# Kernel tuning notes

Measured on AMD Instinct MI355X. Metric: run time of the kernel, lower is better.

Reference implementation:

```python
import jax, jax.numpy as jnp
import numpy as np

B, S, D, H = 2, 2048, 1024, 16
DK = D // H


def setup_inputs() -> dict:
    key = jax.random.key(0)
    ks = jax.random.split(key, 12)
    scale = 0.02
    inp = {
        "query": jax.random.normal(ks[0], (B, S, D), jnp.float32),
        "key_": jax.random.normal(ks[1], (B, S, D), jnp.float32),
        "value": jax.random.normal(ks[2], (B, S, D), jnp.float32),
        # causal mask; masked_fill where mask == 0
        "mask": jnp.tril(jnp.ones((S, S), jnp.int32))[None, None, :, :],
        # torch Linear weights are [out, in]; y = x @ W.T + b
        "Wq": jax.random.normal(ks[3], (D, D), jnp.float32) * scale,
        "bq": jax.random.normal(ks[4], (D,), jnp.float32) * scale,
        "Wk": jax.random.normal(ks[5], (D, D), jnp.float32) * scale,
        "bk": jax.random.normal(ks[6], (D,), jnp.float32) * scale,
        "Wv": jax.random.normal(ks[7], (D, D), jnp.float32) * scale,
        "bv": jax.random.normal(ks[8], (D,), jnp.float32) * scale,
        "Wo": jax.random.normal(ks[9], (D, D), jnp.float32) * scale,
        "bo": jax.random.normal(ks[10], (D,), jnp.float32) * scale,
    }
    return inp


def reference(query, key_, value, mask, Wq, bq, Wk, bk, Wv, bv, Wo, bo):
    # projections (torch Linear: x @ W.T + b)
    Q = query @ Wq.T + bq
    K = key_ @ Wk.T + bk
    V = value @ Wv.T + bv
    # [B, S, D] -> [B, H, S, DK]
    Q = Q.reshape(B, S, H, DK).transpose(0, 2, 1, 3)
    K = K.reshape(B, S, H, DK).transpose(0, 2, 1, 3)
    V = V.reshape(B, S, H, DK).transpose(0, 2, 1, 3)
    scores = jnp.einsum("bhqd,bhkd->bhqk", Q, K) / jnp.sqrt(jnp.float32(DK))
    scores = jnp.where(mask == 0, jnp.float32(-1e9), scores)
    attn = jax.nn.softmax(scores, axis=-1)
    # dropout is identity in eval mode
    context = jnp.einsum("bhqk,bhkd->bhqd", attn, V)
    context = context.transpose(0, 2, 1, 3).reshape(B, S, D)
    output = context @ Wo.T + bo
    return (output, attn)
```

## Files before the change

### kernel.cpp

```cpp
#include <hip/hip_runtime.h>
#include <hip/hip_bf16.h>

#define BB 2
#define SS 2048
#define DD 1024
#define HH 16

typedef __attribute__((ext_vector_type(8))) short bf16x8;
typedef __attribute__((ext_vector_type(4))) float f32x4;
typedef __attribute__((ext_vector_type(4))) unsigned int u32x4;

__device__ inline unsigned short f2bf(float f) {
  unsigned int u = __float_as_uint(f);
  u += 0x7fff + ((u >> 16) & 1);
  return (unsigned short)(u >> 16);
}

__device__ inline void gll16(const void* g, void* l) {
  __builtin_amdgcn_global_load_lds(
      (const __attribute__((address_space(1))) unsigned int*)g,
      (__attribute__((address_space(3))) unsigned int*)l, 16, 0, 0);
}

__device__ inline int swz(int row, int col) {
  return row * 64 + ((((col >> 3) + row + (row >> 3)) & 7) << 3) + (col & 7);
}

__global__ void convert_all(const float* __restrict__ q, const float* __restrict__ k,
                            const float* __restrict__ v, const float* __restrict__ wq,
                            const float* __restrict__ wk, const float* __restrict__ wv,
                            const float* __restrict__ wo, unsigned short* __restrict__ dst) {
  int gi = blockIdx.x * 256 + threadIdx.x;
  long base = (long)gi * 4;
  if (base >= 16777216L) return;
  const float* src;
  long off;
  if (base < 12582912L) {
    int a = (int)(base >> 22);
    off = base & 4194303L;
    src = (a == 0) ? q : (a == 1 ? k : v);
  } else {
    long wb = base - 12582912L;
    int a = (int)(wb >> 20);
    off = wb & 1048575L;
    src = (a == 0) ? wq : (a == 1 ? wk : (a == 2 ? wv : wo));
  }
  const float4 f = *(const float4*)(src + off);
  ushort4 o;
  o.x = f2bf(f.x); o.y = f2bf(f.y); o.z = f2bf(f.z); o.w = f2bf(f.w);
  *(ushort4*)(dst + base) = o;
}

template <int OUT_F32>
__global__ __launch_bounds__(256, 3) void gemm_bt(const unsigned short* __restrict__ Aall,
                                                  const unsigned short* __restrict__ Wall,
                                                  const float* __restrict__ b0,
                                                  const float* __restrict__ b1,
                                                  const float* __restrict__ b2,
                                                  void* __restrict__ Call) {
  __shared__ unsigned short As[128 * 64];
  __shared__ unsigned short Bs[128 * 64];
  const int tid = threadIdx.x;
  const int lane = tid & 63;
  const int w = tid >> 6;
  const int wm = w >> 1, wn = w & 1;
  const int z = blockIdx.z;
  const int m0 = blockIdx.y * 128;
  const int n0 = blockIdx.x * 128;
  const unsigned short* A = Aall + (long)z * 4194304;
  const unsigned short* W = Wall + (long)z * 1048576;
  const float* bias = (z == 0) ? b0 : (z == 1 ? b1 : b2);
  const int r = lane & 15, g = lane >> 4;
  const int lrow = lane >> 3;
  const int lcol = (lane & 7) * 8;

  f32x4 acc[4][4];
#pragma unroll
  for (int i = 0; i < 4; i++)
#pragma unroll
    for (int j = 0; j < 4; j++) acc[i][j] = (f32x4){0.f, 0.f, 0.f, 0.f};

  for (int kt = 0; kt < 16; kt++) {
    const int k0 = kt * 64;
#pragma unroll
    for (int t = 0; t < 4; t++) {
      int row = w * 32 + t * 8 + lrow;
      gll16(A + (long)(m0 + row) * 1024 + k0 + lcol, &As[(w * 32 + t * 8) * 64]);
      gll16(W + (long)(n0 + row) * 1024 + k0 + lcol, &Bs[(w * 32 + t * 8) * 64]);
    }
    __syncthreads();
#pragma unroll
    for (int kk = 0; kk < 2; kk++) {
      bf16x8 af[4], bfr[4];
#pragma unroll
      for (int mi = 0; mi < 4; mi++)
        af[mi] = *(const bf16x8*)&As[(wm * 64 + mi * 16 + r) * 64 + kk * 32 + g * 8];
#pragma unroll
      for (int ni = 0; ni < 4; ni++)
        bfr[ni] = *(const bf16x8*)&Bs[(wn * 64 + ni * 16 + r) * 64 + kk * 32 + g * 8];
#pragma unroll
      for (int mi = 0; mi < 4; mi++)
#pragma unroll
        for (int ni = 0; ni < 4; ni++)
          acc[mi][ni] = __builtin_amdgcn_mfma_f32_16x16x32_bf16(af[mi], bfr[ni], acc[mi][ni], 0, 0, 0);
    }
    __syncthreads();
  }
#pragma unroll
  for (int ni = 0; ni < 4; ni++) {
    int n = n0 + wn * 64 + ni * 16 + r;
    float bv = bias[n];
#pragma unroll
    for (int mi = 0; mi < 4; mi++) {
#pragma unroll
      for (int reg = 0; reg < 4; reg++) {
        int m = m0 + wm * 64 + mi * 16 + g * 4 + reg;
        float val = acc[mi][ni][reg] + bv;
        if (OUT_F32)
          ((float*)Call)[(long)m * 1024 + n] = val;
        else
          ((unsigned short*)Call)[(long)z * 4194304 + (long)m * 1024 + n] = f2bf(val);
      }
    }
  }
}

__global__ __launch_bounds__(256, 4) void attn_kernel(const unsigned short* __restrict__ Qb,
                                                      const unsigned short* __restrict__ Kb,
                                                      const unsigned short* __restrict__ Vb,
                                                      unsigned short* __restrict__ Ctx,
                                                      float* __restrict__ attn) {
  __shared__ unsigned short Qs[64 * 64], Ks[64 * 64], Vt[64 * 64], Ps[64 * 64];
  const int tid = threadIdx.x;
  const int lane = tid & 63;
  const int w = tid >> 6;
  const int r = lane & 15, g = lane >> 4;
  const int qt = blockIdx.x, h = blockIdx.y, b = blockIdx.z;
  const int q0 = qt * 64;
  const int bh = b * HH + h;
  const unsigned short* Qg = Qb + (long)(b * SS + q0) * DD + h * 64;
  const unsigned short* Kg = Kb + (long)b * SS * DD + h * 64;
  const unsigned short* Vg = Vb + (long)b * SS * DD + h * 64;
  float* attn_bh = attn + (long)bh * SS * SS;
  const int srow = tid >> 3;
  const int scg = tid & 7;

#pragma unroll
  for (int it = 0; it < 2; it++) {
    int row = it * 32 + srow;
    u32x4 val = *(const u32x4*)(Qg + (long)row * DD + scg * 8);
    *(u32x4*)&Qs[swz(row, scg * 8)] = val;
  }
  __syncthreads();
  bf16x8 aq0 = *(const bf16x8*)&Qs[swz(16 * w + r, g * 8)];
  bf16x8 aq1 = *(const bf16x8*)&Qs[swz(16 * w + r, 32 + g * 8)];

  float rs[4] = {0.f, 0.f, 0.f, 0.f};
  for (int kt = 0; kt <= qt; kt++) {
    __syncthreads();
#pragma unroll
    for (int it = 0; it < 2; it++) {
      int row = it * 32 + srow;
      u32x4 val = *(const u32x4*)(Kg + (long)(kt * 64 + row) * DD + scg * 8);
      *(u32x4*)&Ks[swz(row, scg * 8)] = val;
    }
    __syncthreads();
#pragma unroll
    for (int tj = 0; tj < 4; tj++) {
      bf16x8 bk0 = *(const bf16x8*)&Ks[swz(tj * 16 + r, g * 8)];
      bf16x8 bk1 = *(const bf16x8*)&Ks[swz(tj * 16 + r, 32 + g * 8)];
      f32x4 sa = (f32x4){0.f, 0.f, 0.f, 0.f};
      sa = __builtin_amdgcn_mfma_f32_16x16x32_bf16(aq0, bk0, sa, 0, 0, 0);
      sa = __builtin_amdgcn_mfma_f32_16x16x32_bf16(aq1, bk1, sa, 0, 0, 0);
      int colb = kt * 64 + tj * 16 + r;
      int rowb = q0 + 16 * w + g * 4;
#pragma unroll
      for (int reg = 0; reg < 4; reg++) {
        float p = (colb <= rowb + reg) ? __expf(sa[reg] * 0.125f) : 0.f;
        rs[reg] += p;
      }
    }
  }
#pragma unroll
  for (int reg = 0; reg < 4; reg++) {
#pragma unroll
    for (int m = 1; m <= 8; m <<= 1) rs[reg] += __shfl_xor(rs[reg], m);
  }
  float inv[4];
#pragma unroll
  for (int reg = 0; reg < 4; reg++) inv[reg] = 1.f / rs[reg];

  f32x4 oacc[4];
#pragma unroll
  for (int dj = 0; dj < 4; dj++) oacc[dj] = (f32x4){0.f, 0.f, 0.f, 0.f};
  for (int kt = 0; kt <= qt; kt++) {
    __syncthreads();
#pragma unroll
    for (int it = 0; it < 2; it++) {
      int row = it * 32 + srow;
      u32x4 val = *(const u32x4*)(Kg + (long)(kt * 64 + row) * DD + scg * 8);
      *(u32x4*)&Ks[swz(row, scg * 8)] = val;
      union { u32x4 v4; unsigned short s[8]; } uv;
      uv.v4 = *(const u32x4*)(Vg + (long)(kt * 64 + row) * DD + scg * 8);
#pragma unroll
      for (int i = 0; i < 8; i++) Vt[swz(scg * 8 + i, row)] = uv.s[i];
    }
    __syncthreads();
#pragma unroll
    for (int tj = 0; tj < 4; tj++) {
      bf16x8 bk0 = *(const bf16x8*)&Ks[swz(tj * 16 + r, g * 8)];
      bf16x8 bk1 = *(const bf16x8*)&Ks[swz(tj * 16 + r, 32 + g * 8)];
      f32x4 sa = (f32x4){0.f, 0.f, 0.f, 0.f};
      sa = __builtin_amdgcn_mfma_f32_16x16x32_bf16(aq0, bk0, sa, 0, 0, 0);
      sa = __builtin_amdgcn_mfma_f32_16x16x32_bf16(aq1, bk1, sa, 0, 0, 0);
      int colb = kt * 64 + tj * 16 + r;
      int rowl = 16 * w + g * 4;
#pragma unroll
      for (int reg = 0; reg < 4; reg++) {
        int rowg = q0 + rowl + reg;
        float p = (colb <= rowg) ? __expf(sa[reg] * 0.125f) * inv[reg] : 0.f;
        attn_bh[(long)rowg * SS + colb] = p;
        Ps[swz(rowl + reg, tj * 16 + r)] = f2bf(p);
      }
    }
    __syncthreads();
#pragma unroll
    for (int kk = 0; kk < 2; kk++) {
      bf16x8 ap = *(const bf16x8*)&Ps[swz(16 * w + r, kk * 32 + g * 8)];
#pragma unroll
      for (int dj = 0; dj < 4; dj++) {
        bf16x8 bv = *(const bf16x8*)&Vt[swz(dj * 16 + r, kk * 32 + g * 8)];
        oacc[dj] = __builtin_amdgcn_mfma_f32_16x16x32_bf16(ap, bv, oacc[dj], 0, 0, 0);
      }
    }
  }
#pragma unroll
  for (int dj = 0; dj < 4; dj++) {
#pragma unroll
    for (int reg = 0; reg < 4; reg++) {
      int rowg = q0 + 16 * w + g * 4 + reg;
      Ctx[(long)(b * SS + rowg) * DD + h * 64 + dj * 16 + r] = f2bf(oacc[dj][reg]);
    }
  }
  int zs = (qt + 1) * 64;
  if (zs < SS) {
    int zc = SS - zs;
    f32x4 zero = (f32x4){0.f, 0.f, 0.f, 0.f};
    for (int rr = 0; rr < 64; rr++) {
      float* rp = attn_bh + (long)(q0 + rr) * SS + zs;
      for (int cc = tid * 4; cc < zc; cc += 1024) *(f32x4*)(rp + cc) = zero;
    }
  }
}

extern "C" void kernel_launch(void* const* d_in, const int* in_sizes, int n_in,
                              void* d_out, int out_size, void* d_ws, size_t ws_size,
                              hipStream_t stream) {
  const float* q  = (const float*)d_in[0];
  const float* k  = (const float*)d_in[1];
  const float* v  = (const float*)d_in[2];
  const float* wq = (const float*)d_in[4];
  const float* bq = (const float*)d_in[5];
  const float* wk = (const float*)d_in[6];
  const float* bk = (const float*)d_in[7];
  const float* wv = (const float*)d_in[8];
  const float* bv = (const float*)d_in[9];
  const float* wo = (const float*)d_in[10];
  const float* bo = (const float*)d_in[11];

  unsigned short* ws = (unsigned short*)d_ws;
  unsigned short* Xq  = ws;
  unsigned short* Wqb = ws + 12582912;
  unsigned short* Qb  = ws + 16777216;
  unsigned short* Ctx = ws + 29360128;
  float* outp = (float*)d_out;
  float* attn = outp + 4194304;

  convert_all<<<dim3(16384), dim3(256), 0, stream>>>(q, k, v, wq, wk, wv, wo, ws);
  gemm_bt<0><<<dim3(8, 32, 3), dim3(256), 0, stream>>>(Xq, Wqb, bq, bk, bv, (void*)Qb);
  attn_kernel<<<dim3(32, 16, 2), dim3(256), 0, stream>>>(Qb, Qb + 4194304, Qb + 8388608, Ctx, attn);
  gemm_bt<1><<<dim3(8, 32, 1), dim3(256), 0, stream>>>(Ctx, Wqb + 3145728, bo, bo, bo, (void*)outp);
}
```

Measured before the change: 815.5 us.

## Pair causal query tiles per block and double-buffer K/V with register prefetch

Each attention block now processes two query tiles, qt and 31-qt, so every block does the same total causal work and there are half as many blocks. K and V tiles are prefetched into registers one iteration ahead and stored into double-buffered shared memory, which removes one barrier per iteration and overlaps global loads with MFMA work. The costs are more shared memory and registers (launch bounds lowered from 4 to 3), fewer blocks in flight, and a tighter sync around the Ps buffer reuse.

```diff
diff --git a/kernel.cpp b/kernel.cpp
--- a/kernel.cpp
+++ b/kernel.cpp
@@ -125,130 +125,152 @@
   }
 }
 
-__global__ __launch_bounds__(256, 4) void attn_kernel(const unsigned short* __restrict__ Qb,
+__global__ __launch_bounds__(256, 3) void attn_kernel(const unsigned short* __restrict__ Qb,
                                                       const unsigned short* __restrict__ Kb,
                                                       const unsigned short* __restrict__ Vb,
                                                       unsigned short* __restrict__ Ctx,
                                                       float* __restrict__ attn) {
-  __shared__ unsigned short Qs[64 * 64], Ks[64 * 64], Vt[64 * 64], Ps[64 * 64];
+  __shared__ unsigned short Qs[64 * 64];
+  __shared__ unsigned short Ks[2][64 * 64];
+  __shared__ unsigned short Vt[2][64 * 64];
+  __shared__ unsigned short Ps[64 * 64];
   const int tid = threadIdx.x;
   const int lane = tid & 63;
   const int w = tid >> 6;
   const int r = lane & 15, g = lane >> 4;
-  const int qt = blockIdx.x, h = blockIdx.y, b = blockIdx.z;
-  const int q0 = qt * 64;
+  const int h = blockIdx.y, b = blockIdx.z;
   const int bh = b * HH + h;
-  const unsigned short* Qg = Qb + (long)(b * SS + q0) * DD + h * 64;
   const unsigned short* Kg = Kb + (long)b * SS * DD + h * 64;
   const unsigned short* Vg = Vb + (long)b * SS * DD + h * 64;
   float* attn_bh = attn + (long)bh * SS * SS;
   const int srow = tid >> 3;
   const int scg = tid & 7;
 
-#pragma unroll
-  for (int it = 0; it < 2; it++) {
-    int row = it * 32 + srow;
-    u32x4 val = *(const u32x4*)(Qg + (long)row * DD + scg * 8);
-    *(u32x4*)&Qs[swz(row, scg * 8)] = val;
-  }
-  __syncthreads();
-  bf16x8 aq0 = *(const bf16x8*)&Qs[swz(16 * w + r, g * 8)];
-  bf16x8 aq1 = *(const bf16x8*)&Qs[swz(16 * w + r, 32 + g * 8)];
-
-  float rs[4] = {0.f, 0.f, 0.f, 0.f};
-  for (int kt = 0; kt <= qt; kt++) {
-    __syncthreads();
+  for (int half = 0; half < 2; half++) {
+    const int qt = half ? (31 - (int)blockIdx.x) : (int)blockIdx.x;
+    const int q0 = qt * 64;
+    const unsigned short* Qg = Qb + (long)(b * SS + q0) * DD + h * 64;
+
+    __syncthreads();
+    u32x4 kpre[2];
 #pragma unroll
     for (int it = 0; it < 2; it++) {
       int row = it * 32 + srow;
-      u32x4 val = *(const u32x4*)(Kg + (long)(kt * 64 + row) * DD + scg * 8);
-      *(u32x4*)&Ks[swz(row, scg * 8)] = val;
-    }
-    __syncthreads();
-#pragma unroll
-    for (int tj = 0; tj < 4; tj++) {
-      bf16x8 bk0 = *(const bf16x8*)&Ks[swz(tj * 16 + r, g * 8)];
-      bf16x8 bk1 = *(const bf16x8*)&Ks[swz(tj * 16 + r, 32 + g * 8)];
-      f32x4 sa = (f32x4){0.f, 0.f, 0.f, 0.f};
-      sa = __builtin_amdgcn_mfma_f32_16x16x32_bf16(aq0, bk0, sa, 0, 0, 0);
-      sa = __builtin_amdgcn_mfma_f32_16x16x32_bf16(aq1, bk1, sa, 0, 0, 0);
-      int colb = kt * 64 + tj * 16 + r;
-      int rowb = q0 + 16 * w + g * 4;
-#pragma unroll
-      for (int reg = 0; reg < 4; reg++) {
-        float p = (colb <= rowb + reg) ? __expf(sa[reg] * 0.125f) : 0.f;
-        rs[reg] += p;
-      }
-    }
-  }
-#pragma unroll
-  for (int reg = 0; reg < 4; reg++) {
-#pragma unroll
-    for (int m = 1; m <= 8; m <<= 1) rs[reg] += __shfl_xor(rs[reg], m);
-  }
-  float inv[4];
-#pragma unroll
-  for (int reg = 0; reg < 4; reg++) inv[reg] = 1.f / rs[reg];
-
-  f32x4 oacc[4];
-#pragma unroll
-  for (int dj = 0; dj < 4; dj++) oacc[dj] = (f32x4){0.f, 0.f, 0.f, 0.f};
-  for (int kt = 0; kt <= qt; kt++) {
-    __syncthreads();
+      *(u32x4*)&Qs[swz(row, scg * 8)] = *(const u32x4*)(Qg + (long)row * DD + scg * 8);
+      kpre[it] = *(const u32x4*)(Kg + (long)row * DD + scg * 8);
+    }
+    __syncthreads();
+    bf16x8 aq0 = *(const bf16x8*)&Qs[swz(16 * w + r, g * 8)];
+    bf16x8 aq1 = *(const bf16x8*)&Qs[swz(16 * w + r, 32 + g * 8)];
+
+    float rs[4] = {0.f, 0.f, 0.f, 0.f};
+    for (int kt = 0; kt <= qt; kt++) {
+      unsigned short* kbuf = Ks[kt & 1];
+#pragma unroll
+      for (int it = 0; it < 2; it++)
+        *(u32x4*)&kbuf[swz(it * 32 + srow, scg * 8)] = kpre[it];
+      const int ktn = (kt < qt) ? kt + 1 : kt;
+#pragma unroll
+      for (int it = 0; it < 2; it++)
+        kpre[it] = *(const u32x4*)(Kg + (long)(ktn * 64 + it * 32 + srow) * DD + scg * 8);
+      __syncthreads();
+#pragma unroll
+      for (int tj = 0; tj < 4; tj++) {
+        bf16x8 bk0 = *(const bf16x8*)&kbuf[swz(tj * 16 + r, g * 8)];
+        bf16x8 bk1 = *(const bf16x8*)&kbuf[swz(tj * 16 + r, 32 + g * 8)];
+        f32x4 sa = (f32x4){0.f, 0.f, 0.f, 0.f};
+        sa = __builtin_amdgcn_mfma_f32_16x16x32_bf16(aq0, bk0, sa, 0, 0, 0);
+        sa = __builtin_amdgcn_mfma_f32_16x16x32_bf16(aq1, bk1, sa, 0, 0, 0);
+        int colb = kt * 64 + tj * 16 + r;
+        int rowb = q0 + 16 * w + g * 4;
+#pragma unroll
+        for (int reg = 0; reg < 4; reg++) {
+          float p = (colb <= rowb + reg) ? __expf(sa[reg] * 0.125f) : 0.f;
+          rs[reg] += p;
+        }
+      }
+    }
+#pragma unroll
+    for (int reg = 0; reg < 4; reg++) {
+#pragma unroll
+      for (int m = 1; m <= 8; m <<= 1) rs[reg] += __shfl_xor(rs[reg], m);
+    }
+    float inv[4];
+#pragma unroll
+    for (int reg = 0; reg < 4; reg++) inv[reg] = 1.f / rs[reg];
+
+    f32x4 oacc[4];
+#pragma unroll
+    for (int dj = 0; dj < 4; dj++) oacc[dj] = (f32x4){0.f, 0.f, 0.f, 0.f};
+    u32x4 vpre[2];
 #pragma unroll
     for (int it = 0; it < 2; it++) {
       int row = it * 32 + srow;
-      u32x4 val = *(const u32x4*)(Kg + (long)(kt * 64 + row) * DD + scg * 8);
-      *(u32x4*)&Ks[swz(row, scg * 8)] = val;
-      union { u32x4 v4; unsigned short s[8]; } uv;
-      uv.v4 = *(const u32x4*)(Vg + (long)(kt * 64 + row) * DD + scg * 8);
-#pragma unroll
-      for (int i = 0; i < 8; i++) Vt[swz(scg * 8 + i, row)] = uv.s[i];
-    }
-    __syncthreads();
-#pragma unroll
-    for (int tj = 0; tj < 4; tj++) {
-      bf16x8 bk0 = *(const bf16x8*)&Ks[swz(tj * 16 + r, g * 8)];
-      bf16x8 bk1 = *(const bf16x8*)&Ks[swz(tj * 16 + r, 32 + g * 8)];
-      f32x4 sa = (f32x4){0.f, 0.f, 0.f, 0.f};
-      sa = __builtin_amdgcn_mfma_f32_16x16x32_bf16(aq0, bk0, sa, 0, 0, 0);
-      sa = __builtin_amdgcn_mfma_f32_16x16x32_bf16(aq1, bk1, sa, 0, 0, 0);
-      int colb = kt * 64 + tj * 16 + r;
-      int rowl = 16 * w + g * 4;
+      kpre[it] = *(const u32x4*)(Kg + (long)row * DD + scg * 8);
+      vpre[it] = *(const u32x4*)(Vg + (long)row * DD + scg * 8);
+    }
+    __syncthreads();
+    for (int kt = 0; kt <= qt; kt++) {
+      unsigned short* kbuf = Ks[kt & 1];
+      unsigned short* vbuf = Vt[kt & 1];
+#pragma unroll
+      for (int it = 0; it < 2; it++) {
+        *(u32x4*)&kbuf[swz(it * 32 + srow, scg * 8)] = kpre[it];
+        union { u32x4 v4; unsigned short s[8]; } uv;
+        uv.v4 = vpre[it];
+#pragma unroll
+        for (int i = 0; i < 8; i++) vbuf[swz(scg * 8 + i, it * 32 + srow)] = uv.s[i];
+      }
+      const int ktn = (kt < qt) ? kt + 1 : kt;
+#pragma unroll
+      for (int it = 0; it < 2; it++) {
+        kpre[it] = *(const u32x4*)(Kg + (long)(ktn * 64 + it * 32 + srow) * DD + scg * 8);
+        vpre[it] = *(const u32x4*)(Vg + (long)(ktn * 64 + it * 32 + srow) * DD + scg * 8);
+      }
+      __syncthreads();
+#pragma unroll
+      for (int tj = 0; tj < 4; tj++) {
+        bf16x8 bk0 = *(const bf16x8*)&kbuf[swz(tj * 16 + r, g * 8)];
+        bf16x8 bk1 = *(const bf16x8*)&kbuf[swz(tj * 16 + r, 32 + g * 8)];
+        f32x4 sa = (f32x4){0.f, 0.f, 0.f, 0.f};
+        sa = __builtin_amdgcn_mfma_f32_16x16x32_bf16(aq0, bk0, sa, 0, 0, 0);
+        sa = __builtin_amdgcn_mfma_f32_16x16x32_bf16(aq1, bk1, sa, 0, 0, 0);
+        int colb = kt * 64 + tj * 16 + r;
+        int rowl = 16 * w + g * 4;
+#pragma unroll
+        for (int reg = 0; reg < 4; reg++) {
+          int rowg = q0 + rowl + reg;
+          float p = (colb <= rowg) ? __expf(sa[reg] * 0.125f) * inv[reg] : 0.f;
+          attn_bh[(long)rowg * SS + colb] = p;
+          Ps[swz(rowl + reg, tj * 16 + r)] = f2bf(p);
+        }
+      }
+#pragma unroll
+      for (int kk = 0; kk < 2; kk++) {
+        bf16x8 ap = *(const bf16x8*)&Ps[swz(16 * w + r, kk * 32 + g * 8)];
+#pragma unroll
+        for (int dj = 0; dj < 4; dj++) {
+          bf16x8 bv = *(const bf16x8*)&vbuf[swz(dj * 16 + r, kk * 32 + g * 8)];
+          oacc[dj] = __builtin_amdgcn_mfma_f32_16x16x32_bf16(ap, bv, oacc[dj], 0, 0, 0);
+        }
+      }
+    }
+#pragma unroll
+    for (int dj = 0; dj < 4; dj++) {
 #pragma unroll
       for (int reg = 0; reg < 4; reg++) {
-        int rowg = q0 + rowl + reg;
-        float p = (colb <= rowg) ? __expf(sa[reg] * 0.125f) * inv[reg] : 0.f;
-        attn_bh[(long)rowg * SS + colb] = p;
-        Ps[swz(rowl + reg, tj * 16 + r)] = f2bf(p);
-      }
-    }
-    __syncthreads();
-#pragma unroll
-    for (int kk = 0; kk < 2; kk++) {
-      bf16x8 ap = *(const bf16x8*)&Ps[swz(16 * w + r, kk * 32 + g * 8)];
-#pragma unroll
-      for (int dj = 0; dj < 4; dj++) {
-        bf16x8 bv = *(const bf16x8*)&Vt[swz(dj * 16 + r, kk * 32 + g * 8)];
-        oacc[dj] = __builtin_amdgcn_mfma_f32_16x16x32_bf16(ap, bv, oacc[dj], 0, 0, 0);
-      }
-    }
-  }
-#pragma unroll
-  for (int dj = 0; dj < 4; dj++) {
-#pragma unroll
-    for (int reg = 0; reg < 4; reg++) {
-      int rowg = q0 + 16 * w + g * 4 + reg;
-      Ctx[(long)(b * SS + rowg) * DD + h * 64 + dj * 16 + r] = f2bf(oacc[dj][reg]);
-    }
-  }
-  int zs = (qt + 1) * 64;
-  if (zs < SS) {
-    int zc = SS - zs;
-    f32x4 zero = (f32x4){0.f, 0.f, 0.f, 0.f};
-    for (int rr = 0; rr < 64; rr++) {
-      float* rp = attn_bh + (long)(q0 + rr) * SS + zs;
-      for (int cc = tid * 4; cc < zc; cc += 1024) *(f32x4*)(rp + cc) = zero;
+        int rowg = q0 + 16 * w + g * 4 + reg;
+        Ctx[(long)(b * SS + rowg) * DD + h * 64 + dj * 16 + r] = f2bf(oacc[dj][reg]);
+      }
+    }
+    int zs = (qt + 1) * 64;
+    if (zs < SS) {
+      int zc = SS - zs;
+      f32x4 zero = (f32x4){0.f, 0.f, 0.f, 0.f};
+      for (int rr = 0; rr < 64; rr++) {
+        float* rp = attn_bh + (long)(q0 + rr) * SS + zs;
+        for (int cc = tid * 4; cc < zc; cc += 1024) *(f32x4*)(rp + cc) = zero;
+      }
     }
   }
 }
@@ -278,6 +300,6 @@
 
   convert_all<<<dim3(16384), dim3(256), 0, stream>>>(q, k, v, wq, wk, wv, wo, ws);
   gemm_bt<0><<<dim3(8, 32, 3), dim3(256), 0, stream>>>(Xq, Wqb, bq, bk, bv, (void*)Qb);
-  attn_kernel<<<dim3(32, 16, 2), dim3(256), 0, stream>>>(Qb, Qb + 4194304, Qb + 8388608, Ctx, attn);
+  attn_kernel<<<dim3(16, 16, 2), dim3(256), 0, stream>>>(Qb, Qb + 4194304, Qb + 8388608, Ctx, attn);
   gemm_bt<1><<<dim3(8, 32, 1), dim3(256), 0, stream>>>(Ctx, Wqb + 3145728, bo, bo, bo, (void*)outp);
 }
```

New measurement: 775.0 us. 5.0% less time.
